# Optimization experiments

Hardware: AMD Instinct MI355X
Metric: run time of the kernel (lower is better)

The kernel has to match this reference:

```python
import jax, jax.numpy as jnp
import numpy as np

B, S, D = 8, 4096, 512      # batch, seq_len, input_dim
H = 2048                    # expert hidden dim
O = 512                     # expert_output_dim
E = 8                       # num_experts
TOP_K = 1


def setup_inputs() -> dict:
    key = jax.random.key(0)
    ks = jax.random.split(key, 8)
    sc = 0.02
    return {
        "x": jax.random.normal(ks[0], (B, S, D), dtype=jnp.float32),
        "Wr": jax.random.normal(ks[1], (D, E), dtype=jnp.float32) * sc,
        "br": jnp.zeros((E,), dtype=jnp.float32),
        "W1": jax.random.normal(ks[2], (E, D, H), dtype=jnp.float32) * sc,
        "b1": jnp.zeros((E, H), dtype=jnp.float32),
        "W2": jax.random.normal(ks[3], (E, H, O), dtype=jnp.float32) * sc,
        "b2": jnp.zeros((E, O), dtype=jnp.float32),
    }


def reference(x, Wr, br, W1, b1, W2, b2):
    b, s, d = x.shape
    xf = x.reshape(-1, d)                                   # [T, D]
    router_logits = xf @ Wr + br                            # [T, E]
    topk_logits, topk_idx = jax.lax.top_k(router_logits, TOP_K)  # [T, K]
    topk_gates = jax.nn.softmax(topk_logits, axis=1)        # [T, K] (ones for K=1)

    out = jnp.zeros((xf.shape[0], O), dtype=x.dtype)
    for k in range(TOP_K):
        idx_k = topk_idx[:, k]                              # [T]
        gate_k = topk_gates[:, k:k + 1]                     # [T, 1]
        # loop over the small fixed expert set; mask-combine per token
        for e in range(E):
            h = jax.nn.relu(xf @ W1[e] + b1[e])             # [T, H]
            oe = h @ W2[e] + b2[e]                          # [T, O]
            mask = (idx_k == e)[:, None]                    # [T, 1]
            out = out + jnp.where(mask, gate_k * oe, 0.0)
    return out.reshape(b, s, O)
```

## Files before the change

### kernel.cpp

```cpp
#include <hip/hip_runtime.h>
#include <stdint.h>

#define N_TOK 32768
#define D_IN  512
#define H_DIM 2048
#define O_DIM 512
#define N_EXP 8
#define NTILES 272
#define TPX    34

typedef __bf16 bf16x8 __attribute__((ext_vector_type(8)));
typedef float  f32x4  __attribute__((ext_vector_type(4)));
typedef unsigned int u32x4 __attribute__((ext_vector_type(4)));

struct alignas(8) us4 { unsigned short x, y, z, w; };

#define FENCE() asm volatile("" ::: "memory")
#define BAR()   do { FENCE(); __builtin_amdgcn_s_barrier(); FENCE(); } while (0)
#define WAITV0  asm volatile("s_waitcnt vmcnt(0)" ::: "memory")

__device__ __forceinline__ unsigned short f2bf(float f) {
  union { float f; unsigned u; } v; v.f = f;
  unsigned r = v.u + 0x7FFFu + ((v.u >> 16) & 1u);
  return (unsigned short)(r >> 16);
}

__device__ __forceinline__ void gll16(const void* src, void* lds_dst) {
  __builtin_amdgcn_global_load_lds(
      (const __attribute__((address_space(1))) void*)src,
      (__attribute__((address_space(3))) void*)lds_dst, 16, 0, 0);
}

__global__ void k_init(int* counts) {
  if (threadIdx.x < N_EXP) counts[threadIdx.x] = 0;
}

__global__ void k_transpose(const float* __restrict__ W, unsigned short* __restrict__ WT,
                            int R, int C) {
  __shared__ unsigned short tile[64][72];
  int e = blockIdx.y;
  const float* src = W + (size_t)e * R * C;
  unsigned short* dst = WT + (size_t)e * R * C;
  int tilesC = C >> 6;
  int tc = (blockIdx.x % tilesC) << 6;
  int tr = (blockIdx.x / tilesC) << 6;
  int tid = threadIdx.x;
  int rq = tid >> 4;
  int cq = tid & 15;
#pragma unroll
  for (int q = 0; q < 4; ++q) {
    int r = q * 16 + rq;
    float4 v = *(const float4*)(src + (size_t)(tr + r) * C + tc + cq * 4);
    us4 b;
    b.x = f2bf(v.x); b.y = f2bf(v.y); b.z = f2bf(v.z); b.w = f2bf(v.w);
    *(us4*)&tile[r][cq * 4] = b;
  }
  __syncthreads();
#pragma unroll
  for (int q = 0; q < 4; ++q) {
    int cc = q * 16 + rq;
    int rr = cq * 4;
    us4 o;
    o.x = tile[rr + 0][cc]; o.y = tile[rr + 1][cc];
    o.z = tile[rr + 2][cc]; o.w = tile[rr + 3][cc];
    *(us4*)(dst + (size_t)(tc + cc) * R + tr + rr) = o;
  }
}

__global__ void k_router(const float* __restrict__ x, const float* __restrict__ Wr,
                         const float* __restrict__ br, int* __restrict__ expert_id,
                         unsigned short* __restrict__ xbf) {
  int token = blockIdx.x * 4 + (threadIdx.x >> 6);
  int lane  = threadIdx.x & 63;
  const float* xr = x + (size_t)token * D_IN;
  float acc[N_EXP];
#pragma unroll
  for (int e = 0; e < N_EXP; ++e) acc[e] = 0.f;
#pragma unroll
  for (int j = 0; j < 2; ++j) {
    int i0 = lane * 8 + j * 4;
    float4 xv = *(const float4*)(xr + i0);
    us4 bb;
    bb.x = f2bf(xv.x); bb.y = f2bf(xv.y); bb.z = f2bf(xv.z); bb.w = f2bf(xv.w);
    *(us4*)(xbf + (size_t)token * D_IN + i0) = bb;
    float xs[4] = {xv.x, xv.y, xv.z, xv.w};
#pragma unroll
    for (int u = 0; u < 4; ++u) {
      const float4* wr = (const float4*)(Wr + (size_t)(i0 + u) * N_EXP);
      float4 w0 = wr[0], w1 = wr[1];
      acc[0] += xs[u] * w0.x; acc[1] += xs[u] * w0.y;
      acc[2] += xs[u] * w0.z; acc[3] += xs[u] * w0.w;
      acc[4] += xs[u] * w1.x; acc[5] += xs[u] * w1.y;
      acc[6] += xs[u] * w1.z; acc[7] += xs[u] * w1.w;
    }
  }
#pragma unroll
  for (int off = 32; off > 0; off >>= 1) {
#pragma unroll
    for (int e = 0; e < N_EXP; ++e) acc[e] += __shfl_xor(acc[e], off, 64);
  }
  if (lane == 0) {
    float best = acc[0] + br[0]; int bi = 0;
#pragma unroll
    for (int e = 1; e < N_EXP; ++e) {
      float v = acc[e] + br[e];
      if (v > best) { best = v; bi = e; }
    }
    expert_id[token] = bi;
  }
}

__global__ void k_count(const int* __restrict__ expert_id, int* __restrict__ counts) {
  __shared__ int lcnt[N_EXP];
  int tid = threadIdx.x;
  if (tid < N_EXP) lcnt[tid] = 0;
  __syncthreads();
  int e = expert_id[blockIdx.x * 1024 + tid];
  atomicAdd(&lcnt[e], 1);
  __syncthreads();
  if (tid < N_EXP) atomicAdd(&counts[tid], lcnt[tid]);
}

__global__ void k_scan(const int* __restrict__ counts, int* __restrict__ offsets,
                       int* __restrict__ cursor, int2* __restrict__ table) {
  int i = threadIdx.x;
  int s = 0, ts = 0, myexp = -1, myt = -1;
#pragma unroll
  for (int e = 0; e < N_EXP; ++e) {
    int c = counts[e];
    int tc = (c + 127) >> 7;
    if (i == e) { offsets[e] = s; cursor[e] = s; }
    if (i >= ts && i < ts + tc) { myexp = e; myt = i - ts; }
    s += c; ts += tc;
  }
  if (i < NTILES) table[i] = make_int2(myexp, myt);
}

__global__ void k_scatter(const int* __restrict__ expert_id, int* __restrict__ cursor,
                          int* __restrict__ idx_list) {
  __shared__ int lcnt[N_EXP], lbase[N_EXP];
  int tid = threadIdx.x;
  int i = blockIdx.x * 512 + tid;
  if (tid < N_EXP) lcnt[tid] = 0;
  __syncthreads();
  int e = expert_id[i];
  int lpos = atomicAdd(&lcnt[e], 1);
  __syncthreads();
  if (tid < N_EXP) lbase[tid] = atomicAdd(&cursor[tid], lcnt[tid]);
  __syncthreads();
  idx_list[lbase[e] + lpos] = i;
}


__launch_bounds__(256, 2)
__global__ void k_gemm1(const unsigned short* __restrict__ xbf,
                        const unsigned short* __restrict__ W1T,
                        const float* __restrict__ b1,
                        const int* __restrict__ counts, const int* __restrict__ offsets,
                        const int2* __restrict__ table, const int* __restrict__ idx_list,
                        unsigned short* __restrict__ Hperm,
                        int nt1, int ch, int hchunk) {
  int xcd = blockIdx.x & 7;
  int s   = blockIdx.x >> 3;
  int tile  = xcd + 8 * (s / nt1);
  int ntile = s % nt1;
  int2 et = table[tile];
  int e = et.x;
  if (e < 0) return;
  int base   = offsets[e] + et.y * 128;
  int mvalid = min(128, counts[e] - et.y * 128);

  __shared__ __align__(16) unsigned char lds[65536];

  int tid = threadIdx.x, w = tid >> 6, lane = tid & 63;
  int l15 = lane & 15, l4 = lane >> 4;
  int wr = w >> 1, wc = w & 1;
  int n0 = ch * hchunk + ntile * 128;

  unsigned offA[4], offB[4];
#pragma unroll
  for (int q = 0; q < 4; ++q) {
    int d   = q * 4096 + w * 1024 + lane * 16;
    int row = d >> 7;
    int bs  = (d & 127) ^ ((row & 7) << 4);
    int tok = idx_list[base + min(row, mvalid - 1)];
    offA[q] = (unsigned)tok * (D_IN * 2) + bs;
    offB[q] = (unsigned)(e * H_DIM + n0 + row) * (D_IN * 2) + bs;
  }

  f32x4 acc[4][4];
#pragma unroll
  for (int a = 0; a < 4; ++a)
#pragma unroll
    for (int b = 0; b < 4; ++b) acc[a][b] = (f32x4){0.f, 0.f, 0.f, 0.f};

#define STAGE1(buf, kstep) do {                                              \
    unsigned kb = (unsigned)(kstep) * 128u;                                  \
    unsigned char* da = lds + (unsigned)(buf) * 16384u;                      \
    unsigned char* db = lds + 32768u + (unsigned)(buf) * 16384u;             \
    _Pragma("unroll")                                                        \
    for (int q = 0; q < 4; ++q) {                                            \
      gll16((const char*)xbf + offA[q] + kb, da + q * 4096 + w * 1024);      \
      gll16((const char*)W1T + offB[q] + kb, db + q * 4096 + w * 1024);      \
    }                                                                        \
  } while (0)

#define COMPUTE1(buf) do {                                                   \
    const unsigned char* A = lds + (unsigned)(buf) * 16384u;                 \
    const unsigned char* B = lds + 32768u + (unsigned)(buf) * 16384u;        \
    __builtin_amdgcn_s_setprio(1);                                           \
    _Pragma("unroll")                                                        \
    for (int ks = 0; ks < 2; ++ks) {                                         \
      int kb = ks * 64 + l4 * 16;                                            \
      bf16x8 bfr[4];                                                         \
      _Pragma("unroll")                                                      \
      for (int nf = 0; nf < 4; ++nf) {                                       \
        int n = wc * 64 + nf * 16 + l15;                                     \
        bfr[nf] = *(const bf16x8*)(B + n * 128 + (kb ^ ((n & 7) << 4)));     \
      }                                                                      \
      _Pragma("unroll")                                                      \
      for (int mf = 0; mf < 4; ++mf) {                                       \
        int m = wr * 64 + mf * 16 + l15;                                     \
        bf16x8 af = *(const bf16x8*)(A + m * 128 + (kb ^ ((m & 7) << 4)));   \
        _Pragma("unroll")                                                    \
        for (int nf = 0; nf < 4; ++nf)                                       \
          acc[mf][nf] = __builtin_amdgcn_mfma_f32_16x16x32_bf16(af, bfr[nf], acc[mf][nf], 0, 0, 0); \
      }                                                                      \
    }                                                                        \
    __builtin_amdgcn_s_setprio(0);                                           \
  } while (0)

  const int NK = D_IN / 64;
  STAGE1(0, 0);
  WAITV0;
  BAR();
  for (int t = 0; t < NK; ++t) {
    if (t + 1 < NK) { STAGE1((t + 1) & 1, t + 1); __builtin_amdgcn_sched_barrier(0); }
    COMPUTE1(t & 1);
    WAITV0;
    BAR();
  }

#pragma unroll
  for (int nf = 0; nf < 4; ++nf) {
    int col = wc * 64 + nf * 16 + l15;
    float bv = b1[(size_t)e * H_DIM + n0 + col];
#pragma unroll
    for (int mf = 0; mf < 4; ++mf) {
#pragma unroll
      for (int j = 0; j < 4; ++j) {
        int row = wr * 64 + mf * 16 + l4 * 4 + j;
        float v = fmaxf(acc[mf][nf][j] + bv, 0.f);
        *(unsigned short*)(lds + row * 256 + ((col * 2) ^ ((row & 7) << 4))) = f2bf(v);
      }
    }
  }
  BAR();
  {
    int row = tid >> 1;
    int seg = (tid & 1) * 128;
    if (row < mvalid) {
      int swz = (row & 7) << 4;
      char* gdst = (char*)Hperm + ((size_t)(base + row) * hchunk + ntile * 128) * 2 + seg;
      const unsigned char* lsrc = lds + row * 256;
#pragma unroll
      for (int i = 0; i < 8; ++i) {
        u32x4 v = *(const u32x4*)(lsrc + ((seg + i * 16) ^ swz));
        *(u32x4*)(gdst + i * 16) = v;
      }
    }
  }
#undef STAGE1
#undef COMPUTE1
}

__launch_bounds__(256, 2)
__global__ void k_gemm2(const unsigned short* __restrict__ Hperm,
                        const unsigned short* __restrict__ W2T,
                        const float* __restrict__ b2,
                        const int* __restrict__ counts, const int* __restrict__ offsets,
                        const int2* __restrict__ table, const int* __restrict__ idx_list,
                        float* __restrict__ out,
                        int ch, int hchunk, int accumulate) {
  int xcd = blockIdx.x & 7;
  int s   = blockIdx.x >> 3;
  int tile  = xcd + 8 * (s >> 2);
  int ntile = s & 3;
  int2 et = table[tile];
  int e = et.x;
  if (e < 0) return;
  int base   = offsets[e] + et.y * 128;
  int mvalid = min(128, counts[e] - et.y * 128);

  __shared__ __align__(16) unsigned char lds[65536];

  int tid = threadIdx.x, w = tid >> 6, lane = tid & 63;
  int l15 = lane & 15, l4 = lane >> 4;
  int wr = w >> 1, wc = w & 1;
  int o0 = ntile * 128;
  const unsigned hrow = (unsigned)hchunk * 2;

  unsigned offA[4], offB[4];
#pragma unroll
  for (int q = 0; q < 4; ++q) {
    int d   = q * 4096 + w * 1024 + lane * 16;
    int row = d >> 7;
    int bs  = (d & 127) ^ ((row & 7) << 4);
    offA[q] = (unsigned)min(base + row, N_TOK - 1) * hrow + bs;
    offB[q] = (unsigned)(e * O_DIM + o0 + row) * (H_DIM * 2) + (unsigned)ch * hchunk * 2 + bs;
  }

  f32x4 acc[4][4];
#pragma unroll
  for (int a = 0; a < 4; ++a)
#pragma unroll
    for (int b = 0; b < 4; ++b) acc[a][b] = (f32x4){0.f, 0.f, 0.f, 0.f};

#define STAGE2(buf, kstep) do {                                              \
    unsigned kb = (unsigned)(kstep) * 128u;                                  \
    unsigned char* da = lds + (unsigned)(buf) * 16384u;                      \
    unsigned char* db = lds + 32768u + (unsigned)(buf) * 16384u;             \
    _Pragma("unroll")                                                        \
    for (int q = 0; q < 4; ++q) {                                            \
      gll16((const char*)Hperm + offA[q] + kb, da + q * 4096 + w * 1024);    \
      gll16((const char*)W2T   + offB[q] + kb, db + q * 4096 + w * 1024);    \
    }                                                                        \
  } while (0)

#define COMPUTE2(buf) do {                                                   \
    const unsigned char* A = lds + (unsigned)(buf) * 16384u;                 \
    const unsigned char* B = lds + 32768u + (unsigned)(buf) * 16384u;        \
    __builtin_amdgcn_s_setprio(1);                                           \
    _Pragma("unroll")                                                        \
    for (int ks = 0; ks < 2; ++ks) {                                         \
      int kb = ks * 64 + l4 * 16;                                            \
      bf16x8 bfr[4];                                                         \
      _Pragma("unroll")                                                      \
      for (int nf = 0; nf < 4; ++nf) {                                       \
        int n = wc * 64 + nf * 16 + l15;                                     \
        bfr[nf] = *(const bf16x8*)(B + n * 128 + (kb ^ ((n & 7) << 4)));     \
      }                                                                      \
      _Pragma("unroll")                                                      \
      for (int mf = 0; mf < 4; ++mf) {                                       \
        int m = wr * 64 + mf * 16 + l15;                                     \
        bf16x8 af = *(const bf16x8*)(A + m * 128 + (kb ^ ((m & 7) << 4)));   \
        _Pragma("unroll")                                                    \
        for (int nf = 0; nf < 4; ++nf)                                       \
          acc[mf][nf] = __builtin_amdgcn_mfma_f32_16x16x32_bf16(af, bfr[nf], acc[mf][nf], 0, 0, 0); \
      }                                                                      \
    }                                                                        \
    __builtin_amdgcn_s_setprio(0);                                           \
  } while (0)

  const int NK = hchunk / 64;
  STAGE2(0, 0);
  WAITV0;
  BAR();
  for (int t = 0; t < NK; ++t) {
    if (t + 1 < NK) { STAGE2((t + 1) & 1, t + 1); __builtin_amdgcn_sched_barrier(0); }
    COMPUTE2(t & 1);
    WAITV0;
    BAR();
  }

#pragma unroll
  for (int nf = 0; nf < 4; ++nf) {
    int o = o0 + wc * 64 + nf * 16 + l15;
    float bv = b2[(size_t)e * O_DIM + o];
#pragma unroll
    for (int mf = 0; mf < 4; ++mf) {
#pragma unroll
      for (int j = 0; j < 4; ++j) {
        int row = wr * 64 + mf * 16 + l4 * 4 + j;
        if (row < mvalid) {
          int tok = idx_list[base + row];
          float* p = out + (size_t)tok * O_DIM + o;
          if (accumulate) *p = *p + acc[mf][nf][j];
          else            *p = acc[mf][nf][j] + bv;
        }
      }
    }
  }
#undef STAGE2
#undef COMPUTE2
}

extern "C" void kernel_launch(void* const* d_in, const int* in_sizes, int n_in,
                              void* d_out, int out_size, void* d_ws, size_t ws_size,
                              hipStream_t stream) {
  const float* x  = (const float*)d_in[0];
  const float* Wr = (const float*)d_in[1];
  const float* br = (const float*)d_in[2];
  const float* W1 = (const float*)d_in[3];
  const float* b1 = (const float*)d_in[4];
  const float* W2 = (const float*)d_in[5];
  const float* b2 = (const float*)d_in[6];
  float* out = (float*)d_out;

  char* ws = (char*)d_ws;
  int*  counts    = (int*)(ws + 0);
  int*  offsets   = (int*)(ws + 64);
  int*  cursor    = (int*)(ws + 128);
  int2* table     = (int2*)(ws + 256);
  int*  expert_id = (int*)(ws + 4096);
  int*  idx_list  = (int*)(ws + 4096 + N_TOK * 4);
  size_t off = 4096 + 2 * (size_t)N_TOK * 4;
  unsigned short* xbf = (unsigned short*)(ws + off);
  off += (size_t)N_TOK * D_IN * 2;
  unsigned short* W1T = (unsigned short*)(ws + off);
  off += (size_t)N_EXP * H_DIM * D_IN * 2;
  unsigned short* W2T = (unsigned short*)(ws + off);
  off += (size_t)N_EXP * H_DIM * O_DIM * 2;
  unsigned short* Hperm = (unsigned short*)(ws + off);

  int hchunk = 2048;
  while (hchunk > 256 && off + (size_t)N_TOK * hchunk * 2 > ws_size) hchunk >>= 1;
  int nch = H_DIM / hchunk;
  int nt1 = hchunk / 128;

  k_init<<<1, 64, 0, stream>>>(counts);
  k_transpose<<<dim3(256, N_EXP), 256, 0, stream>>>(W1, W1T, D_IN, H_DIM);
  k_transpose<<<dim3(256, N_EXP), 256, 0, stream>>>(W2, W2T, H_DIM, O_DIM);
  k_router<<<N_TOK / 4, 256, 0, stream>>>(x, Wr, br, expert_id, xbf);
  k_count<<<N_TOK / 1024, 1024, 0, stream>>>(expert_id, counts);
  k_scan<<<1, 512, 0, stream>>>(counts, offsets, cursor, table);
  k_scatter<<<N_TOK / 512, 512, 0, stream>>>(expert_id, cursor, idx_list);

  for (int ch = 0; ch < nch; ++ch) {
    k_gemm1<<<8 * TPX * nt1, 256, 0, stream>>>(xbf, W1T, b1, counts, offsets,
                                               table, idx_list, Hperm, nt1, ch, hchunk);
    k_gemm2<<<8 * TPX * 4, 256, 0, stream>>>(Hperm, W2T, b2, counts, offsets,
                                             table, idx_list, out, ch, hchunk, ch > 0);
  }
}
```

Baseline: 353.9 us.

## Single-buffer LDS to raise occupancy and make tile-to-XCD mapping contiguous

Both GEMM kernels drop LDS double buffering and go from 64KB to 32KB shared memory, raising launch bounds from 2 to 4 blocks per CU. The goal is to hide load latency through more resident waves instead of software prefetch. The tile index is also changed so each XCD handles a contiguous range of TPX tiles rather than interleaved ones, which should improve L2 locality for expert weights. The cost is that load and compute within one block no longer overlap, and the tighter launch bound may force register spills given the 64-float accumulator.

```diff
diff --git a/kernel.cpp b/kernel.cpp
--- a/kernel.cpp
+++ b/kernel.cpp
@@ -152,7 +152,7 @@
 }
 
 
-__launch_bounds__(256, 2)
+__launch_bounds__(256, 4)
 __global__ void k_gemm1(const unsigned short* __restrict__ xbf,
                         const unsigned short* __restrict__ W1T,
                         const float* __restrict__ b1,
@@ -162,7 +162,7 @@
                         int nt1, int ch, int hchunk) {
   int xcd = blockIdx.x & 7;
   int s   = blockIdx.x >> 3;
-  int tile  = xcd + 8 * (s / nt1);
+  int tile  = xcd * TPX + s / nt1;
   int ntile = s % nt1;
   int2 et = table[tile];
   int e = et.x;
@@ -170,7 +170,7 @@
   int base   = offsets[e] + et.y * 128;
   int mvalid = min(128, counts[e] - et.y * 128);
 
-  __shared__ __align__(16) unsigned char lds[65536];
+  __shared__ __align__(16) unsigned char lds[32768];
 
   int tid = threadIdx.x, w = tid >> 6, lane = tid & 63;
   int l15 = lane & 15, l4 = lane >> 4;
@@ -194,20 +194,18 @@
 #pragma unroll
     for (int b = 0; b < 4; ++b) acc[a][b] = (f32x4){0.f, 0.f, 0.f, 0.f};
 
-#define STAGE1(buf, kstep) do {                                              \
+#define STAGE1(kstep) do {                                                   \
     unsigned kb = (unsigned)(kstep) * 128u;                                  \
-    unsigned char* da = lds + (unsigned)(buf) * 16384u;                      \
-    unsigned char* db = lds + 32768u + (unsigned)(buf) * 16384u;             \
     _Pragma("unroll")                                                        \
     for (int q = 0; q < 4; ++q) {                                            \
-      gll16((const char*)xbf + offA[q] + kb, da + q * 4096 + w * 1024);      \
-      gll16((const char*)W1T + offB[q] + kb, db + q * 4096 + w * 1024);      \
+      gll16((const char*)xbf + offA[q] + kb, lds + q * 4096 + w * 1024);     \
+      gll16((const char*)W1T + offB[q] + kb, lds + 16384 + q * 4096 + w * 1024); \
     }                                                                        \
   } while (0)
 
-#define COMPUTE1(buf) do {                                                   \
-    const unsigned char* A = lds + (unsigned)(buf) * 16384u;                 \
-    const unsigned char* B = lds + 32768u + (unsigned)(buf) * 16384u;        \
+#define COMPUTE1() do {                                                      \
+    const unsigned char* A = lds;                                            \
+    const unsigned char* B = lds + 16384;                                    \
     __builtin_amdgcn_s_setprio(1);                                           \
     _Pragma("unroll")                                                        \
     for (int ks = 0; ks < 2; ++ks) {                                         \
@@ -231,13 +229,11 @@
   } while (0)
 
   const int NK = D_IN / 64;
-  STAGE1(0, 0);
-  WAITV0;
-  BAR();
   for (int t = 0; t < NK; ++t) {
-    if (t + 1 < NK) { STAGE1((t + 1) & 1, t + 1); __builtin_amdgcn_sched_barrier(0); }
-    COMPUTE1(t & 1);
+    STAGE1(t);
     WAITV0;
+    BAR();
+    COMPUTE1();
     BAR();
   }
 
@@ -274,7 +270,7 @@
 #undef COMPUTE1
 }
 
-__launch_bounds__(256, 2)
+__launch_bounds__(256, 4)
 __global__ void k_gemm2(const unsigned short* __restrict__ Hperm,
                         const unsigned short* __restrict__ W2T,
                         const float* __restrict__ b2,
@@ -284,7 +280,7 @@
                         int ch, int hchunk, int accumulate) {
   int xcd = blockIdx.x & 7;
   int s   = blockIdx.x >> 3;
-  int tile  = xcd + 8 * (s >> 2);
+  int tile  = xcd * TPX + (s >> 2);
   int ntile = s & 3;
   int2 et = table[tile];
   int e = et.x;
@@ -292,7 +288,7 @@
   int base   = offsets[e] + et.y * 128;
   int mvalid = min(128, counts[e] - et.y * 128);
 
-  __shared__ __align__(16) unsigned char lds[65536];
+  __shared__ __align__(16) unsigned char lds[32768];
 
   int tid = threadIdx.x, w = tid >> 6, lane = tid & 63;
   int l15 = lane & 15, l4 = lane >> 4;
@@ -316,20 +312,18 @@
 #pragma unroll
     for (int b = 0; b < 4; ++b) acc[a][b] = (f32x4){0.f, 0.f, 0.f, 0.f};
 
-#define STAGE2(buf, kstep) do {                                              \
+#define STAGE2(kstep) do {                                                   \
     unsigned kb = (unsigned)(kstep) * 128u;                                  \
-    unsigned char* da = lds + (unsigned)(buf) * 16384u;                      \
-    unsigned char* db = lds + 32768u + (unsigned)(buf) * 16384u;             \
     _Pragma("unroll")                                                        \
     for (int q = 0; q < 4; ++q) {                                            \
-      gll16((const char*)Hperm + offA[q] + kb, da + q * 4096 + w * 1024);    \
-      gll16((const char*)W2T   + offB[q] + kb, db + q * 4096 + w * 1024);    \
+      gll16((const char*)Hperm + offA[q] + kb, lds + q * 4096 + w * 1024);   \
+      gll16((const char*)W2T   + offB[q] + kb, lds + 16384 + q * 4096 + w * 1024); \
     }                                                                        \
   } while (0)
 
-#define COMPUTE2(buf) do {                                                   \
-    const unsigned char* A = lds + (unsigned)(buf) * 16384u;                 \
-    const unsigned char* B = lds + 32768u + (unsigned)(buf) * 16384u;        \
+#define COMPUTE2() do {                                                      \
+    const unsigned char* A = lds;                                            \
+    const unsigned char* B = lds + 16384;                                    \
     __builtin_amdgcn_s_setprio(1);                                           \
     _Pragma("unroll")                                                        \
     for (int ks = 0; ks < 2; ++ks) {                                         \
@@ -353,13 +347,11 @@
   } while (0)
 
   const int NK = hchunk / 64;
-  STAGE2(0, 0);
-  WAITV0;
-  BAR();
   for (int t = 0; t < NK; ++t) {
-    if (t + 1 < NK) { STAGE2((t + 1) & 1, t + 1); __builtin_amdgcn_sched_barrier(0); }
-    COMPUTE2(t & 1);
+    STAGE2(t);
     WAITV0;
+    BAR();
+    COMPUTE2();
     BAR();
   }
 
```

After: 332.3 us. 1.07x faster.
